# Performance work log

Hardware: AMD Instinct MI355X
Metric: run time of the kernel (lower is better)

The kernel has to match this reference:

```python
import jax, jax.numpy as jnp
import numpy as np


def _hamming(n):
    # torch.hamming_window(n, periodic=False): 0.54 - 0.46*cos(2*pi*i/(n-1))
    if n == 1:
        return jnp.ones((1,), jnp.float32)
    i = jnp.arange(n, dtype=jnp.float32)
    return 0.54 - 0.46 * jnp.cos(2.0 * jnp.pi * i / (n - 1))


def setup_inputs() -> dict:
    key = jax.random.key(0)
    k1, k2, k3 = jax.random.split(key, 3)
    N, CIN, COUT, K = 4, 16, 32, 3
    D, H, W = 16, 64, 64
    x = jax.random.normal(k1, (N, CIN, D, H, W), dtype=jnp.float32)
    # Conv3d default init: U(-1/sqrt(fan_in), 1/sqrt(fan_in)), fan_in = cin*k^3
    bound = 1.0 / np.sqrt(CIN * K * K * K)
    weight = jax.random.uniform(k2, (COUT, CIN, K, K, K), jnp.float32, -bound, bound)
    bias = jax.random.uniform(k3, (COUT,), jnp.float32, -bound, bound)
    gamma = jnp.ones((COUT,), jnp.float32)   # BatchNorm3d weight
    beta = jnp.zeros((COUT,), jnp.float32)   # BatchNorm3d bias
    return {"x": x, "weight": weight, "bias": bias, "gamma": gamma, "beta": beta}


def reference(x, weight, bias, gamma, beta):
    # --- shrink_conv_weights: per-(cout,cin) soft-threshold, fully vectorized ---
    cutoff = weight.max(axis=(2, 3, 4), keepdims=True) * 0.5          # [cout,cin,1,1,1]
    shrunk = jnp.sign(weight) * jax.nn.relu(jnp.abs(weight) - cutoff / 100.0)
    w = jnp.where(weight < cutoff, shrunk, weight)
    # --- hamming window over the 3 kernel dims ---
    kd, kh, kw = w.shape[2], w.shape[3], w.shape[4]
    win = _hamming(kd)[:, None, None] * _hamming(kh)[None, :, None] * _hamming(kw)[None, None, :]
    w = w * win[None, None]                                           # [cout,cin,kd,kh,kw]
    # --- conv3d, padding='same' ---
    y = jax.lax.conv_general_dilated(
        x, w, window_strides=(1, 1, 1), padding="SAME",
        dimension_numbers=("NCDHW", "OIDHW", "NCDHW"))
    y = y + bias[None, :, None, None, None]
    # --- BatchNorm3d (training mode: batch stats, biased variance, eps=1e-5) ---
    mean = y.mean(axis=(0, 2, 3, 4), keepdims=True)
    var = y.var(axis=(0, 2, 3, 4), keepdims=True)
    y = (y - mean) * jax.lax.rsqrt(var + 1e-5)
    y = y * gamma[None, :, None, None, None] + beta[None, :, None, None, None]
    # --- softplus nonlinearity ---
    return jax.nn.softplus(y)
```

## Files before the change

### kernel.cpp

```cpp
#include <hip/hip_runtime.h>
#include <math.h>

#define N_    4
#define CIN   16
#define COUT  32
#define DD    16
#define HH_   64
#define WW_   64
#define MCNT  262144.0f

typedef __attribute__((ext_vector_type(8))) short short8;
typedef __attribute__((ext_vector_type(4))) float floatx4;

__device__ __forceinline__ ushort f2bf(float f) {
    uint u = __float_as_uint(f);
    uint r = (u + 0x7fffu + ((u >> 16) & 1u)) >> 16;
    return (ushort)r;
}
__device__ __forceinline__ float bf2f(ushort v) {
    return __uint_as_float(((uint)v) << 16);
}
__device__ __forceinline__ float softplus_f(float z) {
    return fmaxf(z, 0.0f) + log1pf(expf(-fabsf(z)));
}

#define FAST_XT_F    0
#define FAST_WB_F    2162688
#define FAST_SC_F    2169856
#define FAST_PART_F  2169920
#define FAST_YB_F    2235456
#define FAST_BYTES_FP32Y  ((size_t)FAST_YB_F * 4)
#define FAST_BYTES_BF16Y  ((size_t)(FAST_YB_F + 4194304) * 4)
#define XROW_U16     1056
#define XROW_CHUNKS  132

__global__ __launch_bounds__(256, 4)
void transpose_prep(const float* __restrict__ x, const float* __restrict__ weight,
                    ushort* __restrict__ xt, ushort* __restrict__ wb) {
    __shared__ ushort lds[4 * 64 * 16];
    int b = blockIdx.x;
    int n = b >> 8, d = (b >> 4) & 15, h0 = (b & 15) * 4;
    int t = threadIdx.x;

    if (b == 0) {
        #pragma unroll
        for (int rep = 0; rep < 2; ++rep) {
            int p = t + rep * 256;
            int cout = p >> 4, cin = p & 15;
            const float* wp = weight + (cout * CIN + cin) * 27;
            float wv[27];
            float mx = -INFINITY;
            #pragma unroll
            for (int k = 0; k < 27; ++k) { wv[k] = wp[k]; mx = fmaxf(mx, wv[k]); }
            float cutoff = mx * 0.5f;
            const float win[3] = {0.08f, 1.0f, 0.08f};
            #pragma unroll
            for (int k = 0; k < 27; ++k) {
                float w = wv[k];
                float sg = (w > 0.0f) ? 1.0f : ((w < 0.0f) ? -1.0f : 0.0f);
                float shr = sg * fmaxf(fabsf(w) - cutoff * 0.01f, 0.0f);
                float o = (w < cutoff) ? shr : w;
                int kd = k / 9, kr = k % 9, kh = kr / 3, kw = kr % 3;
                o *= win[kd] * win[kh] * win[kw];
                int q = (kd * 3 + kh) * 3 + kw;
                int grp = q >> 1, half = q & 1;
                wb[(grp * COUT + cout) * 32 + half * 16 + cin] = f2bf(o);
            }
            wb[(13 * COUT + cout) * 32 + 16 + cin] = 0;
        }
    }

    int hh = t >> 6, w = t & 63;
    const float* xp = x + ((size_t)(n * CIN * DD + d) * HH_ + (h0 + hh)) * WW_ + w;
    const int CSTRIDE = DD * HH_ * WW_;
    uint rowv[8];
    #pragma unroll
    for (int cp = 0; cp < 8; ++cp) {
        float a  = xp[(2 * cp)     * CSTRIDE];
        float b2 = xp[(2 * cp + 1) * CSTRIDE];
        rowv[cp] = (uint)f2bf(a) | ((uint)f2bf(b2) << 16);
    }
    #pragma unroll
    for (int cp = 0; cp < 8; ++cp)
        *(uint*)&lds[(hh * 64 + w) * 16 + 2 * cp] = rowv[cp];
    __syncthreads();
    uint* xtg = (uint*)xt;
    for (int i = t; i < 4 * 528; i += 256) {
        int hh2 = i / 528, u = i - hh2 * 528;
        int slot = u >> 3, cp = u & 7;
        uint val = 0;
        if (slot >= 1 && slot <= 64)
            val = *(uint*)&lds[(hh2 * 64 + (slot - 1)) * 16 + 2 * cp];
        xtg[(size_t)((n * DD + d) * HH_ + (h0 + hh2)) * 528 + u] = val;
    }
}

template <int YBF16>
__global__ __launch_bounds__(512, 4)
void conv_mfma_t(const ushort* __restrict__ xt, const ushort* __restrict__ wb,
                 const float* __restrict__ bias, float* __restrict__ outf,
                 ushort* __restrict__ yb, float* __restrict__ part) {
    __shared__ ushort xs[18 * XROW_U16];
    __shared__ float sred[8][64];

    int b = blockIdx.x;
    int n = b >> 8, d = (b >> 4) & 15, h0 = (b & 15) * 4;
    int t = threadIdx.x;
    int l = t & 63;
    int wv_ = t >> 6;
    int hq = wv_ >> 1, cf = wv_ & 1;
    int h = h0 + hq;
    int s = l & 15, g = l >> 4;
    int ghi = g >> 1;

    ((float*)sred)[t] = 0.0f;

    short8 A[14];
    #pragma unroll
    for (int grp = 0; grp < 14; ++grp)
        A[grp] = *(const short8*)&wb[(grp * COUT + cf * 16 + s) * 32 + g * 8];

    const uint4* xt4 = (const uint4*)xt;
    uint4* xs4 = (uint4*)xs;
    for (int i = t; i < 18 * XROW_CHUNKS; i += 512) {
        int row = i / XROW_CHUNKS, c = i - row * XROW_CHUNKS;
        int zdi = row / 6, rh = row - zdi * 6;
        int zd = d - 1 + zdi, zh = h0 - 1 + rh;
        uint4 v = {0u, 0u, 0u, 0u};
        if ((unsigned)zd < DD && (unsigned)zh < HH_)
            v = xt4[(size_t)((n * DD + zd) * HH_ + zh) * XROW_CHUNKS + c];
        xs4[i] = v;
    }
    __syncthreads();

    floatx4 acc[4];
    #pragma unroll
    for (int wf = 0; wf < 4; ++wf) acc[wf] = (floatx4){0.f, 0.f, 0.f, 0.f};

    int hbase = hq * XROW_U16 + s * 16 + (g & 1) * 8;

    #pragma unroll
    for (int grp = 0; grp < 14; ++grp) {
        const int qa = 2 * grp;
        const int qb = (grp == 13) ? 26 : 2 * grp + 1;
        const int t9a = qa / 3, t9b = qb / 3;
        const int ca = ((t9a / 3) * 6 + (t9a % 3)) * XROW_U16 + (qa % 3) * 16;
        const int cb = ((t9b / 3) * 6 + (t9b % 3)) * XROW_U16 + (qb % 3) * 16;
        int baddr = hbase + (ghi ? cb : ca);
        #pragma unroll
        for (int wf = 0; wf < 4; ++wf) {
            short8 B = *(const short8*)&xs[baddr + wf * 256];
            acc[wf] = __builtin_amdgcn_mfma_f32_16x16x32_bf16(A[grp], B, acc[wf], 0, 0, 0);
        }
    }

    float s1[4], s2[4];
    #pragma unroll
    for (int j = 0; j < 4; ++j) { s1[j] = 0.f; s2[j] = 0.f; }
    #pragma unroll
    for (int j = 0; j < 4; ++j) {
        int co = cf * 16 + g * 4 + j;
        float bval = bias[co];
        size_t obase = ((size_t)(n * COUT + co) * DD + d) * (HH_ * WW_) + h * WW_ + s;
        #pragma unroll
        for (int wf = 0; wf < 4; ++wf) {
            float val = acc[wf][j] + bval;
            if (YBF16) yb[obase + wf * 16] = f2bf(val);
            else       outf[obase + wf * 16] = val;
            s1[j] += val;
            s2[j] += val * val;
        }
    }
    #pragma unroll
    for (int m = 1; m < 16; m <<= 1) {
        #pragma unroll
        for (int j = 0; j < 4; ++j) {
            s1[j] += __shfl_xor(s1[j], m);
            s2[j] += __shfl_xor(s2[j], m);
        }
    }
    if (s == 0) {
        #pragma unroll
        for (int j = 0; j < 4; ++j) {
            int co = cf * 16 + g * 4 + j;
            sred[wv_][co]      = s1[j];
            sred[wv_][32 + co] = s2[j];
        }
    }
    __syncthreads();
    if (t < 64) {
        int cfh = (t >> 4) & 1;
        float v = sred[cfh][t] + sred[2 + cfh][t] + sred[4 + cfh][t] + sred[6 + cfh][t];
        part[(size_t)b * 64 + t] = v;
    }
}

__global__ __launch_bounds__(1024)
void stats_fast(const float* __restrict__ part, const float* __restrict__ gamma,
                const float* __restrict__ beta, float* __restrict__ scale,
                float* __restrict__ shift) {
    __shared__ float red[16][64];
    __shared__ float tot[64];
    int t = threadIdx.x;
    int c = t & 63, rg = t >> 6;
    const float* p = part + (size_t)rg * 64 * 64 + c;
    float s = 0.f;
    #pragma unroll 8
    for (int b = 0; b < 64; ++b) s += p[b * 64];
    red[rg][c] = s;
    __syncthreads();
    if (t < 64) {
        float v = 0.f;
        #pragma unroll
        for (int r = 0; r < 16; ++r) v += red[r][t];
        tot[t] = v;
    }
    __syncthreads();
    if (t < 32) {
        float mean = tot[t] / MCNT;
        float var  = tot[32 + t] / MCNT - mean * mean;
        float rstd = rsqrtf(var + 1e-5f);
        float sc = gamma[t] * rstd;
        scale[t] = sc;
        shift[t] = beta[t] - mean * sc;
    }
}

__global__ __launch_bounds__(256)
void bn_act_bf16(const ushort* __restrict__ yb, float* __restrict__ out,
                 const float* __restrict__ scale, const float* __restrict__ shift) {
    const int NV8 = (N_ * COUT * DD * HH_ * WW_) / 8;
    int stride = gridDim.x * blockDim.x;
    const short8* y8 = (const short8*)yb;
    for (int i = blockIdx.x * blockDim.x + threadIdx.x; i < NV8; i += stride) {
        int ch = (i >> 13) & 31;
        float sc = scale[ch];
        float sh = shift[ch];
        short8 yv = y8[i];
        float4 o0, o1;
        float* op0 = (float*)&o0;
        float* op1 = (float*)&o1;
        #pragma unroll
        for (int j = 0; j < 4; ++j) {
            float z = bf2f((ushort)yv[j]) * sc + sh;
            op0[j] = softplus_f(z);
        }
        #pragma unroll
        for (int j = 0; j < 4; ++j) {
            float z = bf2f((ushort)yv[4 + j]) * sc + sh;
            op1[j] = softplus_f(z);
        }
        *(float4*)&out[(size_t)i * 8]     = o0;
        *(float4*)&out[(size_t)i * 8 + 4] = o1;
    }
}

__global__ void bn_act_kernel(float* __restrict__ out, const float* __restrict__ scale,
                              const float* __restrict__ shift) {
    const int NV4 = (N_ * COUT * DD * HH_ * WW_) / 4;
    int stride = gridDim.x * blockDim.x;
    float4* o4 = (float4*)out;
    for (int i = blockIdx.x * blockDim.x + threadIdx.x; i < NV4; i += stride) {
        int ch = (i >> 14) & 31;
        float sc = scale[ch];
        float sh = shift[ch];
        float4 val = o4[i];
        float* vp = (float*)&val;
        #pragma unroll
        for (int j = 0; j < 4; ++j) {
            float z = vp[j] * sc + sh;
            vp[j] = softplus_f(z);
        }
        o4[i] = val;
    }
}

#define WS_W      0
#define WS_SUM    13824
#define WS_SUMSQ  13856
#define WS_SCALE  13888
#define WS_SHIFT  13920

__global__ void prep_weights(const float* __restrict__ weight, float* __restrict__ ws) {
    int t = threadIdx.x;
    if (t < 64) ws[WS_SUM + t] = 0.0f;
    int cout = t >> 4, cin = t & 15;
    const float* wp = weight + (cout * CIN + cin) * 27;
    float wv[27];
    float mx = -INFINITY;
    #pragma unroll
    for (int k = 0; k < 27; ++k) { wv[k] = wp[k]; mx = fmaxf(mx, wv[k]); }
    float cutoff = mx * 0.5f;
    const float win[3] = {0.08f, 1.0f, 0.08f};
    #pragma unroll
    for (int k = 0; k < 27; ++k) {
        float w = wv[k];
        float s = (w > 0.0f) ? 1.0f : ((w < 0.0f) ? -1.0f : 0.0f);
        float shr = s * fmaxf(fabsf(w) - cutoff * 0.01f, 0.0f);
        float o = (w < cutoff) ? shr : w;
        int kd = k / 9, kr = k % 9, kh = kr / 3, kw = kr % 3;
        o *= win[kd] * win[kh] * win[kw];
        ws[WS_W + (cin * 27 + k) * COUT + cout] = o;
    }
}

#define RS 68
__global__ __launch_bounds__(256, 4)
void conv_kernel(const float* __restrict__ x, const float* __restrict__ bias,
                 const float* __restrict__ wsw, float* __restrict__ out,
                 float* __restrict__ sums, float* __restrict__ sumsqs) {
    __shared__ float xsf[3 * 6 * RS];
    __shared__ float sredf[16][8];
    int b = blockIdx.x;
    int n  = b >> 8;
    int d  = (b >> 4) & 15;
    int h0 = (b & 15) << 2;
    int tid = threadIdx.x;
    int wg = tid & 15;
    int cg2 = (tid >> 4) & 3;
    int v  = tid >> 6;
    int cohalf = v & 1;
    int hhalf  = v >> 1;
    int w0 = wg * 4;
    int co0 = cohalf * 16 + cg2 * 4;
    float acc[4][2][4];
    #pragma unroll
    for (int c = 0; c < 4; ++c)
        #pragma unroll
        for (int i = 0; i < 2; ++i)
            #pragma unroll
            for (int j = 0; j < 4; ++j) acc[c][i][j] = 0.0f;
    const float* xn = x + (size_t)n * CIN * DD * HH_ * WW_;
    for (int cin = 0; cin < CIN; ++cin) {
        __syncthreads();
        const float* xc = xn + cin * DD * HH_ * WW_;
        for (int idx = tid; idx < 3 * 6 * RS; idx += 256) {
            int row = idx / RS;
            int c   = idx - row * RS;
            int dd  = row / 6;
            int r   = row - dd * 6;
            int zd = d - 1 + dd;
            int zh = h0 - 1 + r;
            int w  = c - 1;
            float val = 0.0f;
            if ((unsigned)zd < DD && (unsigned)zh < HH_ && (unsigned)w < WW_)
                val = xc[(zd * HH_ + zh) * WW_ + w];
            xsf[idx] = val;
        }
        __syncthreads();
        const float* wc = wsw + cin * 27 * COUT + co0;
        #pragma unroll 1
        for (int kd = 0; kd < 3; ++kd) {
            float4 wvv[9];
            #pragma unroll
            for (int j = 0; j < 9; ++j)
                wvv[j] = *(const float4*)&wc[(kd * 9 + j) * COUT];
            const float* xp = &xsf[(kd * 6 + hhalf * 2) * RS];
            #pragma unroll
            for (int rr = 0; rr < 4; ++rr) {
                const float* xr_ = &xp[rr * RS + w0];
                float4 xm = *(const float4*)xr_;
                float x4 = xr_[4];
                float x5 = xr_[5];
                float xv[6] = {xm.x, xm.y, xm.z, xm.w, x4, x5};
                #pragma unroll
                for (int kh = 0; kh < 3; ++kh) {
                    int i = rr - kh;
                    if (i < 0 || i > 1) continue;
                    #pragma unroll
                    for (int kw = 0; kw < 3; ++kw) {
                        float4 w4 = wvv[kh * 3 + kw];
                        #pragma unroll
                        for (int j = 0; j < 4; ++j) {
                            float xx = xv[j + kw];
                            acc[0][i][j] = fmaf(w4.x, xx, acc[0][i][j]);
                            acc[1][i][j] = fmaf(w4.y, xx, acc[1][i][j]);
                            acc[2][i][j] = fmaf(w4.z, xx, acc[2][i][j]);
                            acc[3][i][j] = fmaf(w4.w, xx, acc[3][i][j]);
                        }
                    }
                }
            }
        }
    }
    float s1[4], s2[4];
    #pragma unroll
    for (int c = 0; c < 4; ++c) {
        float bval = bias[co0 + c];
        s1[c] = 0.0f; s2[c] = 0.0f;
        #pragma unroll
        for (int i = 0; i < 2; ++i) {
            float4 o;
            float* op = (float*)&o;
            #pragma unroll
            for (int j = 0; j < 4; ++j) {
                float val = acc[c][i][j] + bval;
                op[j] = val;
                s1[c] += val;
                s2[c] += val * val;
            }
            int hh = h0 + hhalf * 2 + i;
            *(float4*)&out[((((size_t)n * COUT + co0 + c) * DD + d) * HH_ + hh) * WW_ + w0] = o;
        }
    }
    #pragma unroll
    for (int m = 1; m < 16; m <<= 1) {
        #pragma unroll
        for (int c = 0; c < 4; ++c) {
            s1[c] += __shfl_xor(s1[c], m);
            s2[c] += __shfl_xor(s2[c], m);
        }
    }
    if ((tid & 15) == 0) {
        int gg = tid >> 4;
        #pragma unroll
        for (int c = 0; c < 4; ++c) { sredf[gg][c] = s1[c]; sredf[gg][4 + c] = s2[c]; }
    }
    __syncthreads();
    if (tid < 64) {
        int co   = tid & 31;
        int kind = tid >> 5;
        int ch   = (co >> 4) & 1;
        int cgg  = (co >> 2) & 3;
        int c    = co & 3;
        float val = sredf[ch * 4 + cgg][kind * 4 + c] + sredf[(ch + 2) * 4 + cgg][kind * 4 + c];
        atomicAdd(kind ? &sumsqs[co] : &sums[co], val);
    }
}

__global__ void stats_kernel(const float* __restrict__ gamma, const float* __restrict__ beta,
                             const float* __restrict__ sums, const float* __restrict__ sumsqs,
                             float* __restrict__ scale, float* __restrict__ shift) {
    int c = threadIdx.x;
    if (c >= 32) return;
    float mean = sums[c] / MCNT;
    float var  = sumsqs[c] / MCNT - mean * mean;
    float rstd = rsqrtf(var + 1e-5f);
    float sc = gamma[c] * rstd;
    scale[c] = sc;
    shift[c] = beta[c] - mean * sc;
}

extern "C" void kernel_launch(void* const* d_in, const int* in_sizes, int n_in,
                              void* d_out, int out_size, void* d_ws, size_t ws_size,
                              hipStream_t stream) {
    const float* x      = (const float*)d_in[0];
    const float* weight = (const float*)d_in[1];
    const float* bias   = (const float*)d_in[2];
    const float* gamma  = (const float*)d_in[3];
    const float* beta   = (const float*)d_in[4];
    float* out = (float*)d_out;
    float* wsf = (float*)d_ws;

    if (ws_size >= FAST_BYTES_FP32Y) {
        ushort* xt  = (ushort*)(wsf + FAST_XT_F);
        ushort* wb  = (ushort*)(wsf + FAST_WB_F);
        float* scale = wsf + FAST_SC_F;
        float* shift = wsf + FAST_SC_F + 32;
        float* part  = wsf + FAST_PART_F;
        ushort* yb   = (ushort*)(wsf + FAST_YB_F);

        hipLaunchKernelGGL(transpose_prep, dim3(1024), dim3(256), 0, stream,
                           x, weight, xt, wb);
        if (ws_size >= FAST_BYTES_BF16Y) {
            hipLaunchKernelGGL((conv_mfma_t<1>), dim3(1024), dim3(512), 0, stream,
                               xt, wb, bias, out, yb, part);
            hipLaunchKernelGGL(stats_fast, dim3(1), dim3(1024), 0, stream,
                               part, gamma, beta, scale, shift);
            hipLaunchKernelGGL(bn_act_bf16, dim3(2048), dim3(256), 0, stream,
                               yb, out, scale, shift);
        } else {
            hipLaunchKernelGGL((conv_mfma_t<0>), dim3(1024), dim3(512), 0, stream,
                               xt, wb, bias, out, yb, part);
            hipLaunchKernelGGL(stats_fast, dim3(1), dim3(1024), 0, stream,
                               part, gamma, beta, scale, shift);
            hipLaunchKernelGGL(bn_act_kernel, dim3(2048), dim3(256), 0, stream,
                               out, scale, shift);
        }
    } else {
        hipLaunchKernelGGL(prep_weights, dim3(1), dim3(512), 0, stream, weight, wsf);
        hipLaunchKernelGGL(conv_kernel, dim3(1024), dim3(256), 0, stream,
                           x, bias, wsf + WS_W, out, wsf + WS_SUM, wsf + WS_SUMSQ);
        hipLaunchKernelGGL(stats_kernel, dim3(1), dim3(64), 0, stream,
                           gamma, beta, wsf + WS_SUM, wsf + WS_SUMSQ, wsf + WS_SCALE, wsf + WS_SHIFT);
        hipLaunchKernelGGL(bn_act_kernel, dim3(2048), dim3(256), 0, stream,
                           out, wsf + WS_SCALE, wsf + WS_SHIFT);
    }
}
```

Baseline: 61.67 us.

## Fuse input transpose and weight prep into the MFMA conv kernel

Drops the separate transpose_prep pass. The new conv kernel reads fp32 x directly, converts it to bf16 and packs it channel-interleaved into LDS, and each block also recomputes the shrunk, windowed weights into LDS. This removes one kernel launch and the write and re-read of the bf16 transposed input in global memory. In exchange, every block redoes the weight preprocessing, neighbouring blocks re-read overlapping halo rows of x with strided per-channel loads, and the kernel uses more LDS per block, which may lower occupancy.

```diff
diff --git a/kernel.cpp b/kernel.cpp
--- a/kernel.cpp
+++ b/kernel.cpp
@@ -33,6 +33,207 @@
 #define FAST_BYTES_BF16Y  ((size_t)(FAST_YB_F + 4194304) * 4)
 #define XROW_U16     1056
 #define XROW_CHUNKS  132
+#define WROW_U16     40
+
+__global__ __launch_bounds__(512, 4)
+void conv_direct(const float* __restrict__ x, const float* __restrict__ weight,
+                 const float* __restrict__ bias, ushort* __restrict__ yb,
+                 float* __restrict__ part) {
+    __shared__ ushort xs[18 * XROW_U16];
+    __shared__ ushort wlds[14 * COUT * WROW_U16];
+    __shared__ float sred[8][64];
+
+    int b = blockIdx.x;
+    int n = b >> 8, d = (b >> 4) & 15, h0 = (b & 15) * 4;
+    int t = threadIdx.x;
+    int l = t & 63;
+    int wv_ = t >> 6;
+    int hq = wv_ >> 1, cf = wv_ & 1;
+    int h = h0 + hq;
+    int s = l & 15, g = l >> 4;
+    int ghi = g >> 1;
+
+    ((float*)sred)[t] = 0.0f;
+
+    {
+        int cout = t >> 4, cin = t & 15;
+        const float* wp = weight + (cout * CIN + cin) * 27;
+        float wv[27];
+        float mx = -INFINITY;
+        #pragma unroll
+        for (int k = 0; k < 27; ++k) { wv[k] = wp[k]; mx = fmaxf(mx, wv[k]); }
+        float cutoff = mx * 0.5f;
+        const float win[3] = {0.08f, 1.0f, 0.08f};
+        #pragma unroll
+        for (int k = 0; k < 27; ++k) {
+            float w = wv[k];
+            float sg = (w > 0.0f) ? 1.0f : ((w < 0.0f) ? -1.0f : 0.0f);
+            float shr = sg * fmaxf(fabsf(w) - cutoff * 0.01f, 0.0f);
+            float o = (w < cutoff) ? shr : w;
+            int kd = k / 9, kr = k % 9, kh = kr / 3, kw = kr % 3;
+            o *= win[kd] * win[kh] * win[kw];
+            int q = (kd * 3 + kh) * 3 + kw;
+            int grp = q >> 1, half = q & 1;
+            wlds[(grp * COUT + cout) * WROW_U16 + half * 16 + cin] = f2bf(o);
+        }
+        wlds[(13 * COUT + cout) * WROW_U16 + 16 + cin] = 0;
+    }
+
+    for (int i = t; i < 18 * 2; i += 512) {
+        int row = i >> 1, cq = i & 1;
+        uint4 z = {0u, 0u, 0u, 0u};
+        *(uint4*)&xs[row * XROW_U16 + 0 * 16 + cq * 8]  = z;
+        *(uint4*)&xs[row * XROW_U16 + 65 * 16 + cq * 8] = z;
+    }
+    const int CSTRIDE = DD * HH_ * WW_;
+    for (int i = t; i < 2304; i += 512) {
+        int row = i >> 7;
+        int rem = i & 127;
+        int cq = rem >> 6;
+        int w  = rem & 63;
+        int zdi = row / 6, rh = row - zdi * 6;
+        int zd = d - 1 + zdi, zh = h0 - 1 + rh;
+        uint4 pk = {0u, 0u, 0u, 0u};
+        if ((unsigned)zd < DD && (unsigned)zh < HH_) {
+            const float* p0 = x + (((size_t)(n * CIN + cq * 8) * DD + zd) * HH_ + zh) * WW_ + w;
+            float v0 = p0[0 * CSTRIDE], v1 = p0[1 * CSTRIDE];
+            float v2 = p0[2 * CSTRIDE], v3 = p0[3 * CSTRIDE];
+            float v4 = p0[4 * CSTRIDE], v5 = p0[5 * CSTRIDE];
+            float v6 = p0[6 * CSTRIDE], v7 = p0[7 * CSTRIDE];
+            pk.x = (uint)f2bf(v0) | ((uint)f2bf(v1) << 16);
+            pk.y = (uint)f2bf(v2) | ((uint)f2bf(v3) << 16);
+            pk.z = (uint)f2bf(v4) | ((uint)f2bf(v5) << 16);
+            pk.w = (uint)f2bf(v6) | ((uint)f2bf(v7) << 16);
+        }
+        *(uint4*)&xs[row * XROW_U16 + (w + 1) * 16 + cq * 8] = pk;
+    }
+    __syncthreads();
+
+    short8 A[14];
+    #pragma unroll
+    for (int grp = 0; grp < 14; ++grp)
+        A[grp] = *(const short8*)&wlds[(grp * COUT + cf * 16 + s) * WROW_U16 + g * 8];
+
+    floatx4 acc[4];
+    #pragma unroll
+    for (int wf = 0; wf < 4; ++wf) acc[wf] = (floatx4){0.f, 0.f, 0.f, 0.f};
+
+    int hbase = hq * XROW_U16 + s * 16 + (g & 1) * 8;
+
+    #pragma unroll
+    for (int grp = 0; grp < 14; ++grp) {
+        const int qa = 2 * grp;
+        const int qb = (grp == 13) ? 26 : 2 * grp + 1;
+        const int t9a = qa / 3, t9b = qb / 3;
+        const int ca = ((t9a / 3) * 6 + (t9a % 3)) * XROW_U16 + (qa % 3) * 16;
+        const int cb = ((t9b / 3) * 6 + (t9b % 3)) * XROW_U16 + (qb % 3) * 16;
+        int baddr = hbase + (ghi ? cb : ca);
+        #pragma unroll
+        for (int wf = 0; wf < 4; ++wf) {
+            short8 B = *(const short8*)&xs[baddr + wf * 256];
+            acc[wf] = __builtin_amdgcn_mfma_f32_16x16x32_bf16(A[grp], B, acc[wf], 0, 0, 0);
+        }
+    }
+
+    float s1[4], s2[4];
+    #pragma unroll
+    for (int j = 0; j < 4; ++j) { s1[j] = 0.f; s2[j] = 0.f; }
+    #pragma unroll
+    for (int j = 0; j < 4; ++j) {
+        int co = cf * 16 + g * 4 + j;
+        float bval = bias[co];
+        size_t obase = ((size_t)(n * COUT + co) * DD + d) * (HH_ * WW_) + h * WW_ + s;
+        #pragma unroll
+        for (int wf = 0; wf < 4; ++wf) {
+            float val = acc[wf][j] + bval;
+            yb[obase + wf * 16] = f2bf(val);
+            s1[j] += val;
+            s2[j] += val * val;
+        }
+    }
+    #pragma unroll
+    for (int m = 1; m < 16; m <<= 1) {
+        #pragma unroll
+        for (int j = 0; j < 4; ++j) {
+            s1[j] += __shfl_xor(s1[j], m);
+            s2[j] += __shfl_xor(s2[j], m);
+        }
+    }
+    if (s == 0) {
+        #pragma unroll
+        for (int j = 0; j < 4; ++j) {
+            int co = cf * 16 + g * 4 + j;
+            sred[wv_][co]      = s1[j];
+            sred[wv_][32 + co] = s2[j];
+        }
+    }
+    __syncthreads();
+    if (t < 64) {
+        int cfh = (t >> 4) & 1;
+        float v = sred[cfh][t] + sred[2 + cfh][t] + sred[4 + cfh][t] + sred[6 + cfh][t];
+        part[(size_t)b * 64 + t] = v;
+    }
+}
+
+__global__ __launch_bounds__(1024)
+void stats_fast(const float* __restrict__ part, const float* __restrict__ gamma,
+                const float* __restrict__ beta, float* __restrict__ scale,
+                float* __restrict__ shift) {
+    __shared__ float red[16][64];
+    __shared__ float tot[64];
+    int t = threadIdx.x;
+    int c = t & 63, rg = t >> 6;
+    const float* p = part + (size_t)rg * 64 * 64 + c;
+    float s = 0.f;
+    #pragma unroll 8
+    for (int b = 0; b < 64; ++b) s += p[b * 64];
+    red[rg][c] = s;
+    __syncthreads();
+    if (t < 64) {
+        float v = 0.f;
+        #pragma unroll
+        for (int r = 0; r < 16; ++r) v += red[r][t];
+        tot[t] = v;
+    }
+    __syncthreads();
+    if (t < 32) {
+        float mean = tot[t] / MCNT;
+        float var  = tot[32 + t] / MCNT - mean * mean;
+        float rstd = rsqrtf(var + 1e-5f);
+        float sc = gamma[t] * rstd;
+        scale[t] = sc;
+        shift[t] = beta[t] - mean * sc;
+    }
+}
+
+__global__ __launch_bounds__(256)
+void bn_act_bf16(const ushort* __restrict__ yb, float* __restrict__ out,
+                 const float* __restrict__ scale, const float* __restrict__ shift) {
+    const int NV8 = (N_ * COUT * DD * HH_ * WW_) / 8;
+    int stride = gridDim.x * blockDim.x;
+    const short8* y8 = (const short8*)yb;
+    for (int i = blockIdx.x * blockDim.x + threadIdx.x; i < NV8; i += stride) {
+        int ch = (i >> 13) & 31;
+        float sc = scale[ch];
+        float sh = shift[ch];
+        short8 yv = y8[i];
+        float4 o0, o1;
+        float* op0 = (float*)&o0;
+        float* op1 = (float*)&o1;
+        #pragma unroll
+        for (int j = 0; j < 4; ++j) {
+            float z = bf2f((ushort)yv[j]) * sc + sh;
+            op0[j] = softplus_f(z);
+        }
+        #pragma unroll
+        for (int j = 0; j < 4; ++j) {
+            float z = bf2f((ushort)yv[4 + j]) * sc + sh;
+            op1[j] = softplus_f(z);
+        }
+        *(float4*)&out[(size_t)i * 8]     = o0;
+        *(float4*)&out[(size_t)i * 8 + 4] = o1;
+    }
+}
 
 __global__ __launch_bounds__(256, 4)
 void transpose_prep(const float* __restrict__ x, const float* __restrict__ weight,
@@ -95,11 +296,10 @@
     }
 }
 
-template <int YBF16>
 __global__ __launch_bounds__(512, 4)
-void conv_mfma_t(const ushort* __restrict__ xt, const ushort* __restrict__ wb,
-                 const float* __restrict__ bias, float* __restrict__ outf,
-                 ushort* __restrict__ yb, float* __restrict__ part) {
+void conv_mfma_f32y(const ushort* __restrict__ xt, const ushort* __restrict__ wb,
+                    const float* __restrict__ bias, float* __restrict__ outf,
+                    float* __restrict__ part) {
     __shared__ ushort xs[18 * XROW_U16];
     __shared__ float sred[8][64];
 
@@ -165,8 +365,7 @@
         #pragma unroll
         for (int wf = 0; wf < 4; ++wf) {
             float val = acc[wf][j] + bval;
-            if (YBF16) yb[obase + wf * 16] = f2bf(val);
-            else       outf[obase + wf * 16] = val;
+            outf[obase + wf * 16] = val;
             s1[j] += val;
             s2[j] += val * val;
         }
@@ -192,66 +391,6 @@
         int cfh = (t >> 4) & 1;
         float v = sred[cfh][t] + sred[2 + cfh][t] + sred[4 + cfh][t] + sred[6 + cfh][t];
         part[(size_t)b * 64 + t] = v;
-    }
-}
-
-__global__ __launch_bounds__(1024)
-void stats_fast(const float* __restrict__ part, const float* __restrict__ gamma,
-                const float* __restrict__ beta, float* __restrict__ scale,
-                float* __restrict__ shift) {
-    __shared__ float red[16][64];
-    __shared__ float tot[64];
-    int t = threadIdx.x;
-    int c = t & 63, rg = t >> 6;
-    const float* p = part + (size_t)rg * 64 * 64 + c;
-    float s = 0.f;
-    #pragma unroll 8
-    for (int b = 0; b < 64; ++b) s += p[b * 64];
-    red[rg][c] = s;
-    __syncthreads();
-    if (t < 64) {
-        float v = 0.f;
-        #pragma unroll
-        for (int r = 0; r < 16; ++r) v += red[r][t];
-        tot[t] = v;
-    }
-    __syncthreads();
-    if (t < 32) {
-        float mean = tot[t] / MCNT;
-        float var  = tot[32 + t] / MCNT - mean * mean;
-        float rstd = rsqrtf(var + 1e-5f);
-        float sc = gamma[t] * rstd;
-        scale[t] = sc;
-        shift[t] = beta[t] - mean * sc;
-    }
-}
-
-__global__ __launch_bounds__(256)
-void bn_act_bf16(const ushort* __restrict__ yb, float* __restrict__ out,
-                 const float* __restrict__ scale, const float* __restrict__ shift) {
-    const int NV8 = (N_ * COUT * DD * HH_ * WW_) / 8;
-    int stride = gridDim.x * blockDim.x;
-    const short8* y8 = (const short8*)yb;
-    for (int i = blockIdx.x * blockDim.x + threadIdx.x; i < NV8; i += stride) {
-        int ch = (i >> 13) & 31;
-        float sc = scale[ch];
-        float sh = shift[ch];
-        short8 yv = y8[i];
-        float4 o0, o1;
-        float* op0 = (float*)&o0;
-        float* op1 = (float*)&o1;
-        #pragma unroll
-        for (int j = 0; j < 4; ++j) {
-            float z = bf2f((ushort)yv[j]) * sc + sh;
-            op0[j] = softplus_f(z);
-        }
-        #pragma unroll
-        for (int j = 0; j < 4; ++j) {
-            float z = bf2f((ushort)yv[4 + j]) * sc + sh;
-            op1[j] = softplus_f(z);
-        }
-        *(float4*)&out[(size_t)i * 8]     = o0;
-        *(float4*)&out[(size_t)i * 8 + 4] = o1;
     }
 }
 
@@ -452,31 +591,29 @@
     float* out = (float*)d_out;
     float* wsf = (float*)d_ws;
 
-    if (ws_size >= FAST_BYTES_FP32Y) {
-        ushort* xt  = (ushort*)(wsf + FAST_XT_F);
-        ushort* wb  = (ushort*)(wsf + FAST_WB_F);
-        float* scale = wsf + FAST_SC_F;
-        float* shift = wsf + FAST_SC_F + 32;
-        float* part  = wsf + FAST_PART_F;
-        ushort* yb   = (ushort*)(wsf + FAST_YB_F);
-
+    float* scale = wsf + FAST_SC_F;
+    float* shift = wsf + FAST_SC_F + 32;
+    float* part  = wsf + FAST_PART_F;
+
+    if (ws_size >= FAST_BYTES_BF16Y) {
+        ushort* yb = (ushort*)(wsf + FAST_YB_F);
+        hipLaunchKernelGGL(conv_direct, dim3(1024), dim3(512), 0, stream,
+                           x, weight, bias, yb, part);
+        hipLaunchKernelGGL(stats_fast, dim3(1), dim3(1024), 0, stream,
+                           part, gamma, beta, scale, shift);
+        hipLaunchKernelGGL(bn_act_bf16, dim3(2048), dim3(256), 0, stream,
+                           yb, out, scale, shift);
+    } else if (ws_size >= FAST_BYTES_FP32Y) {
+        ushort* xt = (ushort*)(wsf + FAST_XT_F);
+        ushort* wb = (ushort*)(wsf + FAST_WB_F);
         hipLaunchKernelGGL(transpose_prep, dim3(1024), dim3(256), 0, stream,
                            x, weight, xt, wb);
-        if (ws_size >= FAST_BYTES_BF16Y) {
-            hipLaunchKernelGGL((conv_mfma_t<1>), dim3(1024), dim3(512), 0, stream,
-                               xt, wb, bias, out, yb, part);
-            hipLaunchKernelGGL(stats_fast, dim3(1), dim3(1024), 0, stream,
-                               part, gamma, beta, scale, shift);
-            hipLaunchKernelGGL(bn_act_bf16, dim3(2048), dim3(256), 0, stream,
-                               yb, out, scale, shift);
-        } else {
-            hipLaunchKernelGGL((conv_mfma_t<0>), dim3(1024), dim3(512), 0, stream,
-                               xt, wb, bias, out, yb, part);
-            hipLaunchKernelGGL(stats_fast, dim3(1), dim3(1024), 0, stream,
-                               part, gamma, beta, scale, shift);
-            hipLaunchKernelGGL(bn_act_kernel, dim3(2048), dim3(256), 0, stream,
-                               out, scale, shift);
-        }
+        hipLaunchKernelGGL(conv_mfma_f32y, dim3(1024), dim3(512), 0, stream,
+                           xt, wb, bias, out, part);
+        hipLaunchKernelGGL(stats_fast, dim3(1), dim3(1024), 0, stream,
+                           part, gamma, beta, scale, shift);
+        hipLaunchKernelGGL(bn_act_kernel, dim3(2048), dim3(256), 0, stream,
+                           out, scale, shift);
     } else {
         hipLaunchKernelGGL(prep_weights, dim3(1), dim3(512), 0, stream, weight, wsf);
         hipLaunchKernelGGL(conv_kernel, dim3(1024), dim3(256), 0, stream,
```

Measured after the change: 54.35 us. 11.9% less time.
